# Optimization experiments

Measured on AMD Instinct MI355X. Metric: run time of the kernel, lower is better.

Reference implementation:

```python
import jax, jax.numpy as jnp
import numpy as np

SR = 8000
N_FFT = 800
HOP = 200
N_MELS = 80
N_FREQ = N_FFT // 2 + 1  # 401
STFT_ITER = 50           # InverseMelScale SGD iterations (ctor stft_iter)
GL_ITER = 30             # Griffin-Lim iterations (ctor griflim_iter)
SGD_LR = 0.1             # torchaudio InverseMelScale default sgd lr
SGD_MOM = 0.9            # torchaudio InverseMelScale default sgd momentum
GL_MOM = 0.99            # torchaudio GriffinLim default momentum
POWER = 2.0              # torchaudio GriffinLim default power
TARGET_DB = -0.1


def _mel_fb():
    # torchaudio melscale_fbanks: htk scale, norm=None, f_min=0, f_max=sr/2
    all_freqs = np.linspace(0.0, SR / 2, N_FREQ)
    hz2mel = lambda f: 2595.0 * np.log10(1.0 + f / 700.0)
    mel2hz = lambda m: 700.0 * (10.0 ** (m / 2595.0) - 1.0)
    f_pts = mel2hz(np.linspace(hz2mel(0.0), hz2mel(SR / 2), N_MELS + 2))
    f_diff = f_pts[1:] - f_pts[:-1]
    slopes = f_pts[None, :] - all_freqs[:, None]          # (freq, n_mels+2)
    down = -slopes[:, :-2] / f_diff[:-1]
    up = slopes[:, 2:] / f_diff[1:]
    fb = np.maximum(0.0, np.minimum(down, up))            # (freq, n_mels)
    return jnp.asarray(fb, dtype=jnp.float32)


def _hann(n):
    # torch.hann_window (periodic)
    return (0.5 - 0.5 * jnp.cos(2.0 * jnp.pi * jnp.arange(n) / n)).astype(jnp.float32)


def _frame_idx(n_frames):
    return jnp.arange(n_frames)[:, None] * HOP + jnp.arange(N_FFT)[None, :]


def _stft(x, window):
    # x: (B, L); center=True, reflect pad, onesided -> (B, freq, frames) complex
    pad = N_FFT // 2
    xp = jnp.pad(x, ((0, 0), (pad, pad)), mode='reflect')
    n_frames = 1 + (xp.shape[-1] - N_FFT) // HOP
    frames = xp[:, _frame_idx(n_frames)] * window         # (B, frames, n_fft)
    return jnp.fft.rfft(frames, axis=-1).transpose(0, 2, 1)


def _istft(spec, window):
    # spec: (B, freq, frames) complex -> (B, hop*(frames-1)) real (center trim)
    B, _, n_frames = spec.shape
    frames = jnp.fft.irfft(spec.transpose(0, 2, 1), n=N_FFT, axis=-1) * window
    out_len = N_FFT + HOP * (n_frames - 1)
    idx = _frame_idx(n_frames).reshape(-1)
    y = jnp.zeros((B, out_len), frames.dtype).at[:, idx].add(frames.reshape(B, -1))
    wsq = jnp.zeros((out_len,), window.dtype).at[idx].add(jnp.tile(window ** 2, n_frames))
    y = y / jnp.maximum(wsq, 1e-11)
    pad = N_FFT // 2
    return y[:, pad:out_len - pad]


def _inverse_mel(mel, fb, key):
    # torchaudio InverseMelScale: SGD(momentum) on spec minimizing
    # mean over (B, n_mels) of sum over time of (mel - spec @ fb)^2, clamp >= 0.
    B, M, T = mel.shape
    mel_t = mel.transpose(0, 2, 1)                        # (B, T, M)
    spec0 = jax.random.uniform(key, (B, T, N_FREQ), dtype=jnp.float32)
    scale = 2.0 / (B * M)

    def step(carry, _):
        spec, vel = carry
        diff = mel_t - jnp.einsum('btf,fm->btm', spec, fb)
        g = -scale * jnp.einsum('btm,fm->btf', diff, fb)
        vel = SGD_MOM * vel + g
        spec = jnp.maximum(spec - SGD_LR * vel, 0.0)
        return (spec, vel), None

    (spec, _), _ = jax.lax.scan(step, (spec0, jnp.zeros_like(spec0)), None, length=STFT_ITER)
    return spec.transpose(0, 2, 1)                        # (B, freq, T)


def _griffinlim(spec, key):
    # torchaudio GriffinLim: power=2, momentum=0.99, rand_init complex uniform
    mag = spec ** (1.0 / POWER)                           # (B, freq, T)
    window = _hann(N_FFT)
    kr, ki = jax.random.split(key)
    angles = (jax.random.uniform(kr, spec.shape)
              + 1j * jax.random.uniform(ki, spec.shape)).astype(jnp.complex64)
    beta = GL_MOM / (1.0 + GL_MOM)

    def step(carry, _):
        ang, tprev = carry
        inv = _istft(mag * ang, window)
        rebuilt = _stft(inv, window)
        new = rebuilt - beta * tprev
        new = new / (jnp.abs(new) + 1e-16)
        return (new, rebuilt), None

    (angles, _), _ = jax.lax.scan(step, (angles, jnp.zeros_like(angles)), None, length=GL_ITER)
    return _istft(mag * angles, window)                   # (B, L)


def setup_inputs() -> dict:
    key = jax.random.key(0)
    x = jax.random.uniform(key, (8, N_MELS, 512), dtype=jnp.float32)
    return {'x': x}


def reference(x):
    fb = _mel_fb()
    k1, k2 = jax.random.split(jax.random.key(1))
    spec = _inverse_mel(x.astype(jnp.float32), fb, k1)
    wav = _griffinlim(spec, k2)                           # (B, L)
    # normalize_waveform_batch (vectorized over batch)
    peak = jnp.max(jnp.abs(wav), axis=-1, keepdims=True)
    target_amp = 10.0 ** (TARGET_DB / 20.0)
    wav = wav * (target_amp / peak)
    return wav[:, None, :]                                # (B, 1, L)
```

## Files before the change

### kernel.cpp

```cpp
#include <hip/hip_runtime.h>
#include <math.h>

#define NB 8
#define NMELS 80
#define TT 512
#define NFREQ 401
#define NFFT 800
#define HOPSZ 200
#define NROWS (NB*TT)
#define LY 103000
#define LOUTW 102200
#define PADW 400
#define NSPEC (NROWS*NFREQ)
#define GLITERS 30
#define SGDITERS 50
#define SGD_SCALE 0.003125f
#define KCAT 832
#define KHALF 416
#define NCOLS 448
#define WSQ_SCALE 3276800.0f
#define LO_INV 4.8828125e-4f

#define TWO_PI_D 6.283185307179586476925286766559

typedef _Float16 half8 __attribute__((ext_vector_type(8)));
typedef float f32x4 __attribute__((ext_vector_type(4)));

__host__ __device__ inline void tf2x32(unsigned k0, unsigned k1,
                                       unsigned x0, unsigned x1,
                                       unsigned& o0, unsigned& o1) {
  unsigned ks0 = k0, ks1 = k1, ks2 = k0 ^ k1 ^ 0x1BD11BDAu;
  x0 += ks0; x1 += ks1;
#define TF_R(r) { x0 += x1; x1 = (x1 << (r)) | (x1 >> (32 - (r))); x1 ^= x0; }
  TF_R(13) TF_R(15) TF_R(26) TF_R(6)
  x0 += ks1; x1 += ks2 + 1u;
  TF_R(17) TF_R(29) TF_R(16) TF_R(24)
  x0 += ks2; x1 += ks0 + 2u;
  TF_R(13) TF_R(15) TF_R(26) TF_R(6)
  x0 += ks0; x1 += ks1 + 3u;
  TF_R(17) TF_R(29) TF_R(16) TF_R(24)
  x0 += ks1; x1 += ks2 + 4u;
  TF_R(13) TF_R(15) TF_R(26) TF_R(6)
  x0 += ks2; x1 += ks0 + 5u;
#undef TF_R
  o0 = x0; o1 = x1;
}

__device__ inline float u01(unsigned bits) {
  unsigned u = (bits >> 9) | 0x3f800000u;
  return __uint_as_float(u) - 1.0f;
}

__device__ inline int ang_map(int g) {
  int b = g / (NFREQ * TT);
  int r = g - b * (NFREQ * TT);
  int f = r / TT;
  int t = r - f * TT;
  return (b * TT + t) * NFREQ + f;
}

__global__ void k_rand_spec(unsigned ka, unsigned kb, float* __restrict__ spec) {
  int i = blockIdx.x * blockDim.x + threadIdx.x;
  if (i >= NSPEC) return;
  unsigned o0, o1; tf2x32(ka, kb, 0u, (unsigned)i, o0, o1);
  spec[i] = u01(o0 ^ o1);
}

__global__ void k_rand_ang(unsigned kra, unsigned krb, unsigned kia, unsigned kib,
                           float* __restrict__ ar, float* __restrict__ ai) {
  int g = blockIdx.x * blockDim.x + threadIdx.x;
  if (g >= NSPEC) return;
  int d = ang_map(g);
  unsigned o0, o1;
  tf2x32(kra, krb, 0u, (unsigned)g, o0, o1); ar[d] = u01(o0 ^ o1);
  tf2x32(kia, kib, 0u, (unsigned)g, o0, o1); ai[d] = u01(o0 ^ o1);
}

__device__ inline double mel2hz_d(double mel) {
  return 700.0 * (pow(10.0, mel / 2595.0) - 1.0);
}

__global__ void k_fb(float* __restrict__ fbT, int* __restrict__ fm0,
                     float* __restrict__ fw0, float* __restrict__ fw1) {
  int f = blockIdx.x * blockDim.x + threadIdx.x;
  if (f >= NFREQ) return;
  const double freq = 10.0 * (double)f;
  const double melmax = 2595.0 * log10(1.0 + 4000.0 / 700.0);
  const double step = melmax / 81.0;
  int first = -1; float w0v = 0.f, w1v = 0.f;
  double p0 = 0.0;
  double p1 = mel2hz_d(step);
  for (int m = 0; m < NMELS; ++m) {
    double m2 = (m + 2 == 81) ? melmax : (double)(m + 2) * step;
    double p2 = mel2hz_d(m2);
    double down = (freq - p0) / (p1 - p0);
    double up   = (p2 - freq) / (p2 - p1);
    double v = down < up ? down : up;
    if (v < 0.0) v = 0.0;
    float vf = (float)v;
    fbT[m * NFREQ + f] = vf;
    if (vf > 0.f) {
      if (first < 0) { first = m; w0v = vf; }
      else if (m == first + 1) { w1v = vf; }
    }
    p0 = p1; p1 = p2;
  }
  fm0[f] = first < 0 ? 0 : first;
  fw0[f] = first < 0 ? 0.f : w0v;
  fw1[f] = w1v;
}

__global__ void k_ranges(const float* __restrict__ fbT, int* __restrict__ mlo,
                         int* __restrict__ mhi) {
  int m = threadIdx.x;
  if (m >= NMELS) return;
  int lo = NFREQ, hi = 0;
  for (int f = 0; f < NFREQ; ++f)
    if (fbT[m * NFREQ + f] > 0.f) { if (lo == NFREQ) lo = f; hi = f + 1; }
  mlo[m] = lo; mhi[m] = hi < lo ? lo : hi;
}

__device__ inline double hann_d(int i) {
  return 0.5 - 0.5 * cos(TWO_PI_D * (double)i / 800.0);
}

__global__ void k_wsq(float* __restrict__ wsqs, float* __restrict__ win) {
  int j = blockIdx.x * blockDim.x + threadIdx.x;
  if (j >= LY) return;
  if (j < NFFT) win[j] = (float)hann_d(j);
  int t1 = j / HOPSZ; if (t1 > TT - 1) t1 = TT - 1;
  int t0 = (j - (NFFT - HOPSZ)) / HOPSZ; if (t0 < 0) t0 = 0;
  float s = 0.f;
  for (int t = t0; t <= t1; ++t) {
    float w = (float)hann_d(j - t * HOPSZ);
    s += w * w;
  }
  wsqs[j] = WSQ_SCALE * fmaxf(s, 1e-11f);
}

__global__ void k_tabs1(_Float16* __restrict__ Bh, _Float16* __restrict__ Bl) {
  int idx = blockIdx.x * blockDim.x + threadIdx.x;
  if (idx >= NCOLS * KCAT) return;
  int n = idx / KCAT, kk = idx - n * KCAT;
  double v = 0.0;
  if (n <= 400) {
    if (kk < KHALF) {
      int k = kk;
      if (k <= 400) {
        double ak = (k == 0 || k == 400) ? 1.0 : 2.0;
        int ph = (k * n) % NFFT;
        v = 16.0 * ak * cos((double)ph * (TWO_PI_D / 800.0));
      }
    } else {
      int k = kk - KHALF;
      if (k <= 400) {
        int ph = (k * n) % NFFT;
        v = -32.0 * sin((double)ph * (TWO_PI_D / 800.0));
      }
    }
  }
  float vf = (float)v;
  _Float16 h = (_Float16)vf;
  Bh[idx] = h;
  Bl[idx] = (_Float16)((vf - (float)h) * 2048.0f);
}

__global__ void k_tabs2(_Float16* __restrict__ Bh, _Float16* __restrict__ Bl) {
  int idx = blockIdx.x * blockDim.x + threadIdx.x;
  if (idx >= NCOLS * KCAT) return;
  int kf = idx / KCAT, kk = idx - kf * KCAT;
  double v = 0.0;
  if (kf <= 400) {
    if (kk < KHALF) {
      int nt = kk;
      if (nt <= 400) {
        int ph = (kf * nt) % NFFT;
        v = cos((double)ph * (TWO_PI_D / 800.0));
      }
    } else {
      int nt = kk - KHALF;
      if (nt <= 400) {
        int ph = (kf * nt) % NFFT;
        v = -sin((double)ph * (TWO_PI_D / 800.0));
      }
    }
  }
  float vf = (float)v;
  _Float16 h = (_Float16)vf;
  Bh[idx] = h;
  Bl[idx] = (_Float16)((vf - (float)h) * 2048.0f);
}

__global__ __launch_bounds__(64) void k_sgd(
    const float* __restrict__ spec0, const float* __restrict__ xmel,
    const float* __restrict__ fbT, const int* __restrict__ mlo,
    const int* __restrict__ mhi, const int* __restrict__ fm0,
    const float* __restrict__ fw0, const float* __restrict__ fw1,
    float* __restrict__ mag) {
  __shared__ float s_spec[NFREQ], s_vel[NFREQ], s_diff[NMELS], s_mel[NMELS];
  const int row = blockIdx.x;
  const int b = row / TT, t = row - b * TT;
  const int tid = threadIdx.x;
  for (int f = tid; f < NFREQ; f += 64) { s_spec[f] = spec0[row * NFREQ + f]; s_vel[f] = 0.f; }
  for (int m = tid; m < NMELS; m += 64) s_mel[m] = xmel[(b * NMELS + m) * TT + t];
  __syncthreads();
  for (int it = 0; it < SGDITERS; ++it) {
    for (int m = tid; m < NMELS; m += 64) {
      float acc = 0.f;
      const int lo = mlo[m], hi = mhi[m];
      const float* fr = fbT + m * NFREQ;
      for (int f = lo; f < hi; ++f) acc = fmaf(s_spec[f], fr[f], acc);
      s_diff[m] = s_mel[m] - acc;
    }
    __syncthreads();
    for (int f = tid; f < NFREQ; f += 64) {
      int m0 = fm0[f];
      int m1 = m0 + 1; if (m1 > NMELS - 1) m1 = NMELS - 1;
      float d = s_diff[m0] * fw0[f] + s_diff[m1] * fw1[f];
      float g = -SGD_SCALE * d;
      float v = 0.9f * s_vel[f] + g;
      s_vel[f] = v;
      float sp = s_spec[f] - 0.1f * v;
      s_spec[f] = sp > 0.f ? sp : 0.f;
    }
    __syncthreads();
  }
  for (int f = tid; f < NFREQ; f += 64) mag[row * NFREQ + f] = sqrtf(s_spec[f]);
}

__global__ void k_prep1(const float* __restrict__ mag, const float* __restrict__ ar,
                        const float* __restrict__ ai,
                        _Float16* __restrict__ Ah, _Float16* __restrict__ Al) {
  int kk = blockIdx.x * 256 + threadIdx.x;
  if (kk >= KCAT) return;
  int row = blockIdx.y;
  float v = 0.f;
  if (kk < KHALF) {
    int k = kk;
    if (k <= 400) { int gi = row * NFREQ + k; v = mag[gi] * ar[gi] * 256.0f; }
  } else {
    int k = kk - KHALF;
    if (k <= 400) { int gi = row * NFREQ + k; v = mag[gi] * ai[gi] * 256.0f; }
  }
  _Float16 h = (_Float16)v;
  size_t o = (size_t)row * KCAT + kk;
  Ah[o] = h;
  Al[o] = (_Float16)((v - (float)h) * 2048.0f);
}

#define GEMM_COMPUTE(A0, A1v)                                                   \
  {                                                                             \
    half8 a_h[2], a_l[2];                                                       \
    _Pragma("unroll")                                                           \
    for (int i = 0; i < 2; ++i) {                                               \
      int m = wm * 32 + i * 16 + lm;                                            \
      a_h[i] = *(const half8*)&As_h[m * 40 + qd * 8];                           \
      a_l[i] = *(const half8*)&As_l[m * 40 + qd * 8];                           \
    }                                                                           \
    _Pragma("unroll")                                                           \
    for (int j = 0; j < 2; ++j) {                                               \
      int n = wn * 32 + j * 16 + lm;                                            \
      half8 b_h = *(const half8*)&Bs_h[n * 40 + qd * 8];                        \
      half8 b_l = *(const half8*)&Bs_l[n * 40 + qd * 8];                        \
      _Pragma("unroll")                                                         \
      for (int i = 0; i < 2; ++i) {                                             \
        A0[i][j]  = __builtin_amdgcn_mfma_f32_16x16x32_f16(a_h[i], b_h, A0[i][j], 0, 0, 0);  \
        A1v[i][j] = __builtin_amdgcn_mfma_f32_16x16x32_f16(a_h[i], b_l, A1v[i][j], 0, 0, 0); \
        A1v[i][j] = __builtin_amdgcn_mfma_f32_16x16x32_f16(a_l[i], b_h, A1v[i][j], 0, 0, 0); \
      }                                                                         \
    }                                                                           \
  }

#define GEMM_LOOP                                                               \
  uint4 pa_h = *(const uint4*)&Ah[abase];                                       \
  uint4 pa_l = *(const uint4*)&Al[abase];                                       \
  uint4 pb_h = *(const uint4*)&Bh[bbase];                                       \
  uint4 pb_l = *(const uint4*)&Bl[bbase];                                       \
  for (int c = 0; c < 26; ++c) {                                                \
    *(uint4*)&As_h[sr * 40 + sk] = pa_h;                                        \
    *(uint4*)&As_l[sr * 40 + sk] = pa_l;                                        \
    *(uint4*)&Bs_h[sr * 40 + sk] = pb_h;                                        \
    *(uint4*)&Bs_l[sr * 40 + sk] = pb_l;                                        \
    __syncthreads();                                                            \
    if (c < 25) {                                                               \
      int off = (c + 1) * 32;                                                   \
      pa_h = *(const uint4*)&Ah[abase + off];                                   \
      pa_l = *(const uint4*)&Al[abase + off];                                   \
      pb_h = *(const uint4*)&Bh[bbase + off];                                   \
      pb_l = *(const uint4*)&Bl[bbase + off];                                   \
    }                                                                           \
    if (c < 13) { GEMM_COMPUTE(ac0, ac1) } else { GEMM_COMPUTE(as0, as1) }      \
    __syncthreads();                                                            \
  }

__global__ __launch_bounds__(256, 2) void k_mm1(
    const _Float16* __restrict__ Ah, const _Float16* __restrict__ Al,
    const _Float16* __restrict__ Bh, const _Float16* __restrict__ Bl,
    const float* __restrict__ win, float* __restrict__ frames) {
  __shared__ __align__(16) _Float16 As_h[64 * 40], As_l[64 * 40];
  __shared__ __align__(16) _Float16 Bs_h[64 * 40], Bs_l[64 * 40];
  const int t = threadIdx.x;
  const int row0 = blockIdx.y * 64;
  const int col0 = blockIdx.x * 64;
  const int sr = t >> 2, sk = (t & 3) * 8;
  const int lane = t & 63, wv = t >> 6;
  const int wm = wv & 1, wn = wv >> 1;
  const int lm = lane & 15, qd = lane >> 4;
  f32x4 ac0[2][2] = {}, ac1[2][2] = {}, as0[2][2] = {}, as1[2][2] = {};
  const size_t abase = (size_t)(row0 + sr) * KCAT + sk;
  const size_t bbase = (size_t)(col0 + sr) * KCAT + sk;
  GEMM_LOOP
#pragma unroll
  for (int j = 0; j < 2; ++j) {
    int col = col0 + wn * 32 + j * 16 + lm;
    if (col <= 400) {
      float wA = win[col];
      bool mir = (col >= 1 && col <= 399);
      float wB = mir ? win[800 - col] : 0.f;
#pragma unroll
      for (int i = 0; i < 2; ++i)
#pragma unroll
        for (int r = 0; r < 4; ++r) {
          int row = row0 + wm * 32 + i * 16 + qd * 4 + r;
          float Cv = ac0[i][j][r] + ac1[i][j][r] * LO_INV;
          float Sv = as0[i][j][r] + as1[i][j][r] * LO_INV;
          frames[(size_t)row * NFFT + col] = (Cv + Sv) * wA;
          if (mir) frames[(size_t)row * NFFT + (800 - col)] = (Cv - Sv) * wB;
        }
    }
  }
}

__device__ inline float sample_y(const float* __restrict__ fb_,
                                 const float* __restrict__ wsqs, int j) {
  int jm = (j < PADW) ? (NFFT - j) : ((j < PADW + LOUTW) ? j : (205198 - j));
  int t1 = jm / HOPSZ; if (t1 > TT - 1) t1 = TT - 1;
  int t0 = (jm - (NFFT - HOPSZ)) / HOPSZ; if (t0 < 0) t0 = 0;
  float s = 0.f;
  for (int t = t0; t <= t1; ++t) s += fb_[t * NFFT + (jm - t * HOPSZ)];
  return s / wsqs[jm];
}

__global__ void k_olaprep(const float* __restrict__ frames, const float* __restrict__ wsqs,
                          const float* __restrict__ win,
                          _Float16* __restrict__ A2h, _Float16* __restrict__ A2l) {
  int idx = blockIdx.x * 256 + threadIdx.x;
  if (idx >= NROWS * KHALF) return;
  int row = idx / KHALF, n = idx - row * KHALF;
  size_t ab = (size_t)row * KCAT;
  if (n > 400) {
    A2h[ab + n] = (_Float16)0.f; A2l[ab + n] = (_Float16)0.f;
    A2h[ab + KHALF + n] = (_Float16)0.f; A2l[ab + KHALF + n] = (_Float16)0.f;
    return;
  }
  int b = row >> 9, tt = row & 511;
  const float* fb_ = frames + (size_t)b * TT * NFFT;
  int start = tt * HOPSZ;
  float x1 = sample_y(fb_, wsqs, start + n) * win[n] * 256.0f;
  float x2 = 0.f;
  if (n >= 1 && n <= 399)
    x2 = sample_y(fb_, wsqs, start + 800 - n) * win[800 - n] * 256.0f;
  float E = x1 + x2, O = x1 - x2;
  _Float16 Eh = (_Float16)E;
  A2h[ab + n] = Eh;
  A2l[ab + n] = (_Float16)((E - (float)Eh) * 2048.0f);
  _Float16 Oh = (_Float16)O;
  A2h[ab + KHALF + n] = Oh;
  A2l[ab + KHALF + n] = (_Float16)((O - (float)Oh) * 2048.0f);
}

__global__ __launch_bounds__(256, 2) void k_mm2(
    const _Float16* __restrict__ Ah, const _Float16* __restrict__ Al,
    const _Float16* __restrict__ Bh, const _Float16* __restrict__ Bl,
    const float* __restrict__ mag,
    float* __restrict__ tppr, float* __restrict__ tppi,
    _Float16* __restrict__ A1h, _Float16* __restrict__ A1l, float beta) {
  __shared__ __align__(16) _Float16 As_h[64 * 40], As_l[64 * 40];
  __shared__ __align__(16) _Float16 Bs_h[64 * 40], Bs_l[64 * 40];
  const int t = threadIdx.x;
  const int row0 = blockIdx.y * 64;
  const int col0 = blockIdx.x * 64;
  const int sr = t >> 2, sk = (t & 3) * 8;
  const int lane = t & 63, wv = t >> 6;
  const int wm = wv & 1, wn = wv >> 1;
  const int lm = lane & 15, qd = lane >> 4;
  f32x4 ac0[2][2] = {}, ac1[2][2] = {}, as0[2][2] = {}, as1[2][2] = {};
  const size_t abase = (size_t)(row0 + sr) * KCAT + sk;
  const size_t bbase = (size_t)(col0 + sr) * KCAT + sk;
  GEMM_LOOP
#pragma unroll
  for (int j = 0; j < 2; ++j) {
    int col = col0 + wn * 32 + j * 16 + lm;
    if (col <= 400) {
#pragma unroll
      for (int i = 0; i < 2; ++i)
#pragma unroll
        for (int r = 0; r < 4; ++r) {
          int row = row0 + wm * 32 + i * 16 + qd * 4 + r;
          int idx = row * NFREQ + col;
          float rr = ac0[i][j][r] + ac1[i][j][r] * LO_INV;
          float ri = as0[i][j][r] + as1[i][j][r] * LO_INV;
          float nr = rr - beta * tppr[idx];
          float ni = ri - beta * tppi[idx];
          tppr[idx] = rr; tppi[idx] = ri;
          float den = sqrtf(nr * nr + ni * ni) + 1e-16f;
          float arv = nr / den, aiv = ni / den;
          float mg = mag[idx] * 256.0f;
          size_t ab = (size_t)row * KCAT;
          float v1 = mg * arv;
          _Float16 h1 = (_Float16)v1;
          A1h[ab + col] = h1;
          A1l[ab + col] = (_Float16)((v1 - (float)h1) * 2048.0f);
          float v2 = mg * aiv;
          _Float16 h2 = (_Float16)v2;
          A1h[ab + KHALF + col] = h2;
          A1l[ab + KHALF + col] = (_Float16)((v2 - (float)h2) * 2048.0f);
        }
    }
  }
}

__global__ void k_ola(const float* __restrict__ frames, const float* __restrict__ wsqs,
                      float* __restrict__ y) {
  int idx = blockIdx.x * blockDim.x + threadIdx.x;
  if (idx >= NB * LY) return;
  int b = idx / LY, j = idx - b * LY;
  int t1 = j / HOPSZ; if (t1 > TT - 1) t1 = TT - 1;
  int t0 = (j - (NFFT - HOPSZ)) / HOPSZ; if (t0 < 0) t0 = 0;
  const float* fb_ = frames + (size_t)b * TT * NFFT;
  float s = 0.f;
  for (int t = t0; t <= t1; ++t) s += fb_[t * NFFT + (j - t * HOPSZ)];
  y[idx] = s / wsqs[j];
}

__global__ void k_absmax(const float* __restrict__ y, float* __restrict__ peak) {
  __shared__ float red[256];
  int b = blockIdx.x;
  const float* yb = y + (size_t)b * LY + PADW;
  float mx = 0.f;
  for (int j = threadIdx.x; j < LOUTW; j += 256) mx = fmaxf(mx, fabsf(yb[j]));
  red[threadIdx.x] = mx;
  __syncthreads();
  for (int s2 = 128; s2 > 0; s2 >>= 1) {
    if (threadIdx.x < s2) red[threadIdx.x] = fmaxf(red[threadIdx.x], red[threadIdx.x + s2]);
    __syncthreads();
  }
  if (threadIdx.x == 0) peak[b] = red[0];
}

__global__ void k_scale(const float* __restrict__ y, const float* __restrict__ peak,
                        float* __restrict__ out, float target) {
  int idx = blockIdx.x * blockDim.x + threadIdx.x;
  if (idx >= NB * LOUTW) return;
  int b = idx / LOUTW, j = idx - b * LOUTW;
  out[idx] = y[(size_t)b * LY + PADW + j] * (target / peak[b]);
}

__global__ void k_zero2(float* __restrict__ a, float* __restrict__ b, int n) {
  int i = blockIdx.x * blockDim.x + threadIdx.x;
  if (i < n) { a[i] = 0.f; b[i] = 0.f; }
}

extern "C" void kernel_launch(void* const* d_in, const int* in_sizes, int n_in,
                              void* d_out, int out_size, void* d_ws, size_t ws_size,
                              hipStream_t stream) {
  const float* xmel = (const float*)d_in[0];
  float* out = (float*)d_out;

  char* p = (char*)d_ws;
  auto alloc = [&](size_t nbytes) -> void* {
    void* r = (void*)p;
    p += (nbytes + 255) & ~(size_t)255;
    return r;
  };
  float* mag  = (float*)alloc((size_t)NSPEC * 4);
  float* ar   = (float*)alloc((size_t)NSPEC * 4);
  float* ai   = (float*)alloc((size_t)NSPEC * 4);
  float* tpr  = (float*)alloc((size_t)NSPEC * 4);
  float* tpi  = (float*)alloc((size_t)NSPEC * 4);
  float* y    = (float*)alloc((size_t)NB * LY * 4);
  float* win  = (float*)alloc(NFFT * 4);
  float* wsqs = (float*)alloc((size_t)LY * 4);
  float* fbT  = (float*)alloc((size_t)NMELS * NFREQ * 4);
  float* fw0  = (float*)alloc(NFREQ * 4);
  float* fw1  = (float*)alloc(NFREQ * 4);
  float* peak = (float*)alloc(NB * 4);
  int* fm0    = (int*)alloc(NFREQ * 4);
  int* mlo    = (int*)alloc(NMELS * 4);
  int* mhi    = (int*)alloc(NMELS * 4);
  float* frames = (float*)alloc((size_t)NROWS * NFFT * 4);
  float* spec0 = frames;
  _Float16* A1h = (_Float16*)alloc((size_t)NROWS * KCAT * 2);
  _Float16* A1l = (_Float16*)alloc((size_t)NROWS * KCAT * 2);
  _Float16* A2h = (_Float16*)alloc((size_t)NROWS * KCAT * 2);
  _Float16* A2l = (_Float16*)alloc((size_t)NROWS * KCAT * 2);
  _Float16* B1h = (_Float16*)alloc((size_t)NCOLS * KCAT * 2);
  _Float16* B1l = (_Float16*)alloc((size_t)NCOLS * KCAT * 2);
  _Float16* B2h = (_Float16*)alloc((size_t)NCOLS * KCAT * 2);
  _Float16* B2l = (_Float16*)alloc((size_t)NCOLS * KCAT * 2);

  if ((size_t)(p - (char*)d_ws) > ws_size) return;

  unsigned k1a, k1b, k2a, k2b, kra, krb, kia, kib;
  {
    unsigned o0, o1;
    tf2x32(0u, 1u, 0u, 0u, o0, o1); k1a = o0; k1b = o1;
    tf2x32(0u, 1u, 0u, 1u, o0, o1); k2a = o0; k2b = o1;
    tf2x32(k2a, k2b, 0u, 0u, o0, o1); kra = o0; krb = o1;
    tf2x32(k2a, k2b, 0u, 1u, o0, o1); kia = o0; kib = o1;
  }

  k_fb<<<2, 256, 0, stream>>>(fbT, fm0, fw0, fw1);
  k_ranges<<<1, 128, 0, stream>>>(fbT, mlo, mhi);
  k_wsq<<<(LY + 255) / 256, 256, 0, stream>>>(wsqs, win);
  k_tabs1<<<(NCOLS * KCAT + 255) / 256, 256, 0, stream>>>(B1h, B1l);
  k_tabs2<<<(NCOLS * KCAT + 255) / 256, 256, 0, stream>>>(B2h, B2l);
  k_zero2<<<(NSPEC + 255) / 256, 256, 0, stream>>>(tpr, tpi, NSPEC);
  k_rand_spec<<<(NSPEC + 255) / 256, 256, 0, stream>>>(k1a, k1b, spec0);
  k_rand_ang<<<(NSPEC + 255) / 256, 256, 0, stream>>>(kra, krb, kia, kib, ar, ai);

  k_sgd<<<NROWS, 64, 0, stream>>>(spec0, xmel, fbT, mlo, mhi, fm0, fw0, fw1, mag);

  k_prep1<<<dim3(4, NROWS), 256, 0, stream>>>(mag, ar, ai, A1h, A1l);

  const float beta = (float)(0.99 / 1.99);
  for (int it = 0; it < GLITERS; ++it) {
    k_mm1<<<dim3(7, 64), 256, 0, stream>>>(A1h, A1l, B1h, B1l, win, frames);
    k_olaprep<<<(NROWS * KHALF + 255) / 256, 256, 0, stream>>>(frames, wsqs, win, A2h, A2l);
    k_mm2<<<dim3(7, 64), 256, 0, stream>>>(A2h, A2l, B2h, B2l,
                                           mag, tpr, tpi, A1h, A1l, beta);
  }
  k_mm1<<<dim3(7, 64), 256, 0, stream>>>(A1h, A1l, B1h, B1l, win, frames);
  k_ola<<<(NB * LY + 255) / 256, 256, 0, stream>>>(frames, wsqs, y);

  k_absmax<<<NB, 256, 0, stream>>>(y, peak);
  const float target = (float)pow(10.0, -0.1 / 20.0);
  k_scale<<<(NB * LOUTW + 255) / 256, 256, 0, stream>>>(y, peak, out, target);
}
```

Baseline: 2.713 ms.

## Double-buffer GEMM LDS tiles, register-cache SGD state, precompute inverse window sums

```diff
diff --git a/kernel.cpp b/kernel.cpp
--- a/kernel.cpp
+++ b/kernel.cpp
@@ -18,6 +18,7 @@
 #define KCAT 832
 #define KHALF 416
 #define NCOLS 448
+#define MAXSPAN 24
 #define WSQ_SCALE 3276800.0f
 #define LO_INV 4.8828125e-4f
 
@@ -124,7 +125,8 @@
   return 0.5 - 0.5 * cos(TWO_PI_D * (double)i / 800.0);
 }
 
-__global__ void k_wsq(float* __restrict__ wsqs, float* __restrict__ win) {
+__global__ void k_wsq(float* __restrict__ wsqs, float* __restrict__ wsinv,
+                      float* __restrict__ win) {
   int j = blockIdx.x * blockDim.x + threadIdx.x;
   if (j >= LY) return;
   if (j < NFFT) win[j] = (float)hann_d(j);
@@ -135,7 +137,9 @@
     float w = (float)hann_d(j - t * HOPSZ);
     s += w * w;
   }
-  wsqs[j] = WSQ_SCALE * fmaxf(s, 1e-11f);
+  s = fmaxf(s, 1e-11f);
+  wsqs[j] = WSQ_SCALE * s;
+  wsinv[j] = (float)(1.0 / ((double)WSQ_SCALE * (double)s));
 }
 
 __global__ void k_tabs1(_Float16* __restrict__ Bh, _Float16* __restrict__ Bl) {
@@ -197,35 +201,78 @@
     const int* __restrict__ mhi, const int* __restrict__ fm0,
     const float* __restrict__ fw0, const float* __restrict__ fw1,
     float* __restrict__ mag) {
-  __shared__ float s_spec[NFREQ], s_vel[NFREQ], s_diff[NMELS], s_mel[NMELS];
+  __shared__ float s_spec[NFREQ], s_diff[NMELS];
   const int row = blockIdx.x;
   const int b = row / TT, t = row - b * TT;
   const int tid = threadIdx.x;
-  for (int f = tid; f < NFREQ; f += 64) { s_spec[f] = spec0[row * NFREQ + f]; s_vel[f] = 0.f; }
-  for (int m = tid; m < NMELS; m += 64) s_mel[m] = xmel[(b * NMELS + m) * TT + t];
+
+  float spec[7], vel[7];
+  int qm0[7], qm1[7];
+  float qw0[7], qw1[7];
+#pragma unroll
+  for (int q = 0; q < 7; ++q) {
+    int f = tid + 64 * q;
+    bool v = f < NFREQ;
+    float sv = v ? spec0[row * NFREQ + f] : 0.f;
+    spec[q] = sv; vel[q] = 0.f;
+    if (v) s_spec[f] = sv;
+    int m0 = v ? fm0[f] : 0;
+    int m1 = m0 + 1; if (m1 > NMELS - 1) m1 = NMELS - 1;
+    qm0[q] = m0; qm1[q] = m1;
+    qw0[q] = v ? fw0[f] : 0.f;
+    qw1[q] = v ? fw1[f] : 0.f;
+  }
+
+  const int mA = tid;
+  const int mB = tid + 64;
+  const bool hasB = mB < NMELS;
+  float melA = xmel[(b * NMELS + mA) * TT + t];
+  float melB = hasB ? xmel[(b * NMELS + mB) * TT + t] : 0.f;
+  int loA = mlo[mA];
+  int hiA = mhi[mA];
+  int loB = hasB ? mlo[mB] : 0;
+  int hiB = hasB ? mhi[mB] : 0;
+  float fbA[MAXSPAN], fbB[MAXSPAN];
+#pragma unroll
+  for (int i = 0; i < MAXSPAN; ++i) {
+    fbA[i] = (loA + i < hiA) ? fbT[mA * NFREQ + loA + i] : 0.f;
+    fbB[i] = (hasB && loB + i < hiB) ? fbT[mB * NFREQ + loB + i] : 0.f;
+  }
   __syncthreads();
+
   for (int it = 0; it < SGDITERS; ++it) {
-    for (int m = tid; m < NMELS; m += 64) {
-      float acc = 0.f;
-      const int lo = mlo[m], hi = mhi[m];
-      const float* fr = fbT + m * NFREQ;
-      for (int f = lo; f < hi; ++f) acc = fmaf(s_spec[f], fr[f], acc);
-      s_diff[m] = s_mel[m] - acc;
-    }
+    float accA = 0.f, accB = 0.f;
+#pragma unroll
+    for (int i = 0; i < MAXSPAN; ++i) {
+      int fA = loA + i; if (fA > 400) fA = 400;
+      int fB = loB + i; if (fB > 400) fB = 400;
+      accA = fmaf(fbA[i], s_spec[fA], accA);
+      accB = fmaf(fbB[i], s_spec[fB], accB);
+    }
+    s_diff[mA] = melA - accA;
+    if (hasB) s_diff[mB] = melB - accB;
     __syncthreads();
-    for (int f = tid; f < NFREQ; f += 64) {
-      int m0 = fm0[f];
-      int m1 = m0 + 1; if (m1 > NMELS - 1) m1 = NMELS - 1;
-      float d = s_diff[m0] * fw0[f] + s_diff[m1] * fw1[f];
-      float g = -SGD_SCALE * d;
-      float v = 0.9f * s_vel[f] + g;
-      s_vel[f] = v;
-      float sp = s_spec[f] - 0.1f * v;
-      s_spec[f] = sp > 0.f ? sp : 0.f;
+#pragma unroll
+    for (int q = 0; q < 7; ++q) {
+      int f = tid + 64 * q;
+      if (f < NFREQ) {
+        float d = s_diff[qm0[q]] * qw0[q] + s_diff[qm1[q]] * qw1[q];
+        float g = -SGD_SCALE * d;
+        float v = 0.9f * vel[q] + g;
+        vel[q] = v;
+        float sp = spec[q] - 0.1f * v;
+        sp = sp > 0.f ? sp : 0.f;
+        spec[q] = sp;
+        s_spec[f] = sp;
+      }
     }
     __syncthreads();
   }
-  for (int f = tid; f < NFREQ; f += 64) mag[row * NFREQ + f] = sqrtf(s_spec[f]);
+#pragma unroll
+  for (int q = 0; q < 7; ++q) {
+    int f = tid + 64 * q;
+    if (f < NFREQ) mag[row * NFREQ + f] = sqrtf(spec[q]);
+  }
 }
 
 __global__ void k_prep1(const float* __restrict__ mag, const float* __restrict__ ar,
@@ -248,20 +295,26 @@
   Al[o] = (_Float16)((v - (float)h) * 2048.0f);
 }
 
-#define GEMM_COMPUTE(A0, A1v)                                                   \
+#define GEMM_STAGE(BUF)                                                         \
+    *(uint4*)&As_h[BUF][sr * 40 + sk] = pa_h;                                   \
+    *(uint4*)&As_l[BUF][sr * 40 + sk] = pa_l;                                   \
+    *(uint4*)&Bs_h[BUF][sr * 40 + sk] = pb_h;                                   \
+    *(uint4*)&Bs_l[BUF][sr * 40 + sk] = pb_l;
+
+#define GEMM_COMPUTE(BUF, A0, A1v)                                              \
   {                                                                             \
     half8 a_h[2], a_l[2];                                                       \
     _Pragma("unroll")                                                           \
     for (int i = 0; i < 2; ++i) {                                               \
       int m = wm * 32 + i * 16 + lm;                                            \
-      a_h[i] = *(const half8*)&As_h[m * 40 + qd * 8];                           \
-      a_l[i] = *(const half8*)&As_l[m * 40 + qd * 8];                           \
+      a_h[i] = *(const half8*)&As_h[BUF][m * 40 + qd * 8];                      \
+      a_l[i] = *(const half8*)&As_l[BUF][m * 40 + qd * 8];                      \
     }                                                                           \
     _Pragma("unroll")                                                           \
     for (int j = 0; j < 2; ++j) {                                               \
       int n = wn * 32 + j * 16 + lm;                                            \
-      half8 b_h = *(const half8*)&Bs_h[n * 40 + qd * 8];                        \
-      half8 b_l = *(const half8*)&Bs_l[n * 40 + qd * 8];                        \
+      half8 b_h = *(const half8*)&Bs_h[BUF][n * 40 + qd * 8];                   \
+      half8 b_l = *(const half8*)&Bs_l[BUF][n * 40 + qd * 8];                   \
       _Pragma("unroll")                                                         \
       for (int i = 0; i < 2; ++i) {                                             \
         A0[i][j]  = __builtin_amdgcn_mfma_f32_16x16x32_f16(a_h[i], b_h, A0[i][j], 0, 0, 0);  \
@@ -276,11 +329,9 @@
   uint4 pa_l = *(const uint4*)&Al[abase];                                       \
   uint4 pb_h = *(const uint4*)&Bh[bbase];                                       \
   uint4 pb_l = *(const uint4*)&Bl[bbase];                                       \
+  GEMM_STAGE(0)                                                                 \
+  _Pragma("unroll 2")                                                           \
   for (int c = 0; c < 26; ++c) {                                                \
-    *(uint4*)&As_h[sr * 40 + sk] = pa_h;                                        \
-    *(uint4*)&As_l[sr * 40 + sk] = pa_l;                                        \
-    *(uint4*)&Bs_h[sr * 40 + sk] = pb_h;                                        \
-    *(uint4*)&Bs_l[sr * 40 + sk] = pb_l;                                        \
     __syncthreads();                                                            \
     if (c < 25) {                                                               \
       int off = (c + 1) * 32;                                                   \
@@ -289,16 +340,17 @@
       pb_h = *(const uint4*)&Bh[bbase + off];                                   \
       pb_l = *(const uint4*)&Bl[bbase + off];                                   \
     }                                                                           \
-    if (c < 13) { GEMM_COMPUTE(ac0, ac1) } else { GEMM_COMPUTE(as0, as1) }      \
-    __syncthreads();                                                            \
+    const int bf = c & 1;                                                       \
+    if (c < 13) { GEMM_COMPUTE(bf, ac0, ac1) } else { GEMM_COMPUTE(bf, as0, as1) } \
+    if (c < 25) { GEMM_STAGE(bf ^ 1) }                                          \
   }
 
 __global__ __launch_bounds__(256, 2) void k_mm1(
     const _Float16* __restrict__ Ah, const _Float16* __restrict__ Al,
     const _Float16* __restrict__ Bh, const _Float16* __restrict__ Bl,
     const float* __restrict__ win, float* __restrict__ frames) {
-  __shared__ __align__(16) _Float16 As_h[64 * 40], As_l[64 * 40];
-  __shared__ __align__(16) _Float16 Bs_h[64 * 40], Bs_l[64 * 40];
+  __shared__ __align__(16) _Float16 As_h[2][64 * 40], As_l[2][64 * 40];
+  __shared__ __align__(16) _Float16 Bs_h[2][64 * 40], Bs_l[2][64 * 40];
   const int t = threadIdx.x;
   const int row0 = blockIdx.y * 64;
   const int col0 = blockIdx.x * 64;
@@ -332,16 +384,16 @@
 }
 
 __device__ inline float sample_y(const float* __restrict__ fb_,
-                                 const float* __restrict__ wsqs, int j) {
+                                 const float* __restrict__ wsinv, int j) {
   int jm = (j < PADW) ? (NFFT - j) : ((j < PADW + LOUTW) ? j : (205198 - j));
   int t1 = jm / HOPSZ; if (t1 > TT - 1) t1 = TT - 1;
   int t0 = (jm - (NFFT - HOPSZ)) / HOPSZ; if (t0 < 0) t0 = 0;
   float s = 0.f;
   for (int t = t0; t <= t1; ++t) s += fb_[t * NFFT + (jm - t * HOPSZ)];
-  return s / wsqs[jm];
-}
-
-__global__ void k_olaprep(const float* __restrict__ frames, const float* __restrict__ wsqs,
+  return s * wsinv[jm];
+}
+
+__global__ void k_olaprep(const float* __restrict__ frames, const float* __restrict__ wsinv,
                           const float* __restrict__ win,
                           _Float16* __restrict__ A2h, _Float16* __restrict__ A2l) {
   int idx = blockIdx.x * 256 + threadIdx.x;
@@ -356,10 +408,10 @@
   int b = row >> 9, tt = row & 511;
   const float* fb_ = frames + (size_t)b * TT * NFFT;
   int start = tt * HOPSZ;
-  float x1 = sample_y(fb_, wsqs, start + n) * win[n] * 256.0f;
+  float x1 = sample_y(fb_, wsinv, start + n) * win[n] * 256.0f;
   float x2 = 0.f;
   if (n >= 1 && n <= 399)
-    x2 = sample_y(fb_, wsqs, start + 800 - n) * win[800 - n] * 256.0f;
+    x2 = sample_y(fb_, wsinv, start + 800 - n) * win[800 - n] * 256.0f;
   float E = x1 + x2, O = x1 - x2;
   _Float16 Eh = (_Float16)E;
   A2h[ab + n] = Eh;
@@ -375,8 +427,8 @@
     const float* __restrict__ mag,
     float* __restrict__ tppr, float* __restrict__ tppi,
     _Float16* __restrict__ A1h, _Float16* __restrict__ A1l, float beta) {
-  __shared__ __align__(16) _Float16 As_h[64 * 40], As_l[64 * 40];
-  __shared__ __align__(16) _Float16 Bs_h[64 * 40], Bs_l[64 * 40];
+  __shared__ __align__(16) _Float16 As_h[2][64 * 40], As_l[2][64 * 40];
+  __shared__ __align__(16) _Float16 Bs_h[2][64 * 40], Bs_l[2][64 * 40];
   const int t = threadIdx.x;
   const int row0 = blockIdx.y * 64;
   const int col0 = blockIdx.x * 64;
@@ -481,6 +533,7 @@
   float* y    = (float*)alloc((size_t)NB * LY * 4);
   float* win  = (float*)alloc(NFFT * 4);
   float* wsqs = (float*)alloc((size_t)LY * 4);
+  float* wsinv= (float*)alloc((size_t)LY * 4);
   float* fbT  = (float*)alloc((size_t)NMELS * NFREQ * 4);
   float* fw0  = (float*)alloc(NFREQ * 4);
   float* fw1  = (float*)alloc(NFREQ * 4);
@@ -512,7 +565,7 @@
 
   k_fb<<<2, 256, 0, stream>>>(fbT, fm0, fw0, fw1);
   k_ranges<<<1, 128, 0, stream>>>(fbT, mlo, mhi);
-  k_wsq<<<(LY + 255) / 256, 256, 0, stream>>>(wsqs, win);
+  k_wsq<<<(LY + 255) / 256, 256, 0, stream>>>(wsqs, wsinv, win);
   k_tabs1<<<(NCOLS * KCAT + 255) / 256, 256, 0, stream>>>(B1h, B1l);
   k_tabs2<<<(NCOLS * KCAT + 255) / 256, 256, 0, stream>>>(B2h, B2l);
   k_zero2<<<(NSPEC + 255) / 256, 256, 0, stream>>>(tpr, tpi, NSPEC);
@@ -526,7 +579,7 @@
   const float beta = (float)(0.99 / 1.99);
   for (int it = 0; it < GLITERS; ++it) {
     k_mm1<<<dim3(7, 64), 256, 0, stream>>>(A1h, A1l, B1h, B1l, win, frames);
-    k_olaprep<<<(NROWS * KHALF + 255) / 256, 256, 0, stream>>>(frames, wsqs, win, A2h, A2l);
+    k_olaprep<<<(NROWS * KHALF + 255) / 256, 256, 0, stream>>>(frames, wsinv, win, A2h, A2l);
     k_mm2<<<dim3(7, 64), 256, 0, stream>>>(A2h, A2l, B2h, B2l,
                                            mag, tpr, tpi, A1h, A1l, beta);
   }
```

After: 2.523 ms. -7.0%, faster.
